# Kernel tuning notes

Hardware: AMD Instinct MI355X
Metric: run time of the kernel (lower is better)

## Reference

```python
import jax, jax.numpy as jnp
import numpy as np

B, T, N = 512, 1024, 48


def setup_inputs() -> dict:
    key = jax.random.key(0)
    k1, k2, k3, k4 = jax.random.split(key, 4)
    potentials = jax.random.normal(k1, (B, T, N), dtype=jnp.float32)
    y_true = jax.random.randint(k2, (B, T), 0, N, dtype=jnp.int32)
    lengths = jax.random.randint(k3, (B,), 1, T + 1, dtype=jnp.int32)
    transitions = jax.random.normal(k4, (N, N), dtype=jnp.float32)
    return {"potentials": potentials, "y_true": y_true,
            "lengths": lengths, "transitions": transitions}


def _crf_log_likelihood(potentials, tags, lengths, trans):
    # potentials: [B,T,N], tags: [B,T] int, lengths: [B] int, trans: [N,N]
    Bv, Tv, Nv = potentials.shape
    t_idx = jnp.arange(Tv)

    # ---- numerator: score of the given tag sequence ----
    unary = jnp.take_along_axis(potentials, tags[..., None], axis=2)[..., 0]  # [B,T]
    unary_mask = (t_idx[None, :] < lengths[:, None]).astype(potentials.dtype)
    unary_score = jnp.sum(unary * unary_mask, axis=1)  # [B]

    trans_scores = trans[tags[:, :-1], tags[:, 1:]]  # [B,T-1]
    pair_mask = (t_idx[None, 1:] < lengths[:, None]).astype(potentials.dtype)
    binary_score = jnp.sum(trans_scores * pair_mask, axis=1)  # [B]
    seq_score = unary_score + binary_score

    # ---- log partition: forward algorithm with length masking ----
    alpha0 = potentials[:, 0, :]  # [B,N]
    pots_rest = jnp.transpose(potentials[:, 1:, :], (1, 0, 2))  # [T-1,B,N]
    valid = (t_idx[1:, None] < lengths[None, :])  # [T-1,B]

    def step(alpha, inp):
        pot_t, v = inp  # [B,N], [B]
        # logsumexp over previous state: alpha[b,i] + trans[i,j]
        new_alpha = jax.nn.logsumexp(alpha[:, :, None] + trans[None, :, :], axis=1) + pot_t
        alpha = jnp.where(v[:, None], new_alpha, alpha)
        return alpha, None

    alpha_final, _ = jax.lax.scan(step, alpha0, (pots_rest, valid))
    log_norm = jax.nn.logsumexp(alpha_final, axis=-1)  # [B]

    return seq_score - log_norm


def reference(potentials, y_true, lengths, transitions):
    ll = _crf_log_likelihood(potentials, y_true.astype(jnp.int32),
                             lengths.astype(jnp.int32), transitions)
    return -ll  # per-sample NLL, shape [B]
```

## Files before the change

kernel.cpp:

```cpp
#include <hip/hip_runtime.h>
#include <cstdint>
#include <cstddef>

constexpr int Bb = 512;
constexpr int Tt = 1024;
constexpr int Nn = 48;
constexpr int SG = 16;
constexpr int NG = Bb / SG;
constexpr int Cc = 32;
constexpr int Lc = Tt / Cc;
constexpr int Wb = 32;

typedef short bf16x8 __attribute__((ext_vector_type(8)));
typedef float f32x4  __attribute__((ext_vector_type(4)));
typedef unsigned int u32x4 __attribute__((ext_vector_type(4)));

__device__ __forceinline__ unsigned int bf16_rne(float x) {
    const unsigned int u = __float_as_uint(x);
    return ((u + 0x7FFFu + ((u >> 16) & 1u)) >> 16);
}
__device__ __forceinline__ unsigned int pack2(float lo, float hi) {
    return bf16_rne(lo) | (bf16_rne(hi) << 16);
}
__device__ __forceinline__ float safe_log(float x) {
    return __logf(fmaxf(x, 1e-30f));
}

__launch_bounds__(64, 1)
__global__ void crf_fused(const float* __restrict__ pot,
                          const int*   __restrict__ ytrue,
                          const int*   __restrict__ lengths,
                          const float* __restrict__ trans,
                          float*       __restrict__ out)
{
    __shared__ float trans_lds[Nn * Nn];

    const int lane = threadIdx.x;
    const int ln   = lane & 15;
    const int q    = lane >> 4;
    const int gidx = blockIdx.x >> 5;
    const int c    = blockIdx.x & 31;
    const int s0   = gidx * SG;

    for (int i = lane; i < Nn * Nn; i += 64) trans_lds[i] = trans[i];
    __syncthreads();

    {
        const int    b    = blockIdx.x >> 1;
        const int    h    = blockIdx.x & 1;
        const int    lenb = lengths[b];
        const int*   yrow = ytrue + (size_t)b * Tt;
        const float* prow = pot + (size_t)b * Tt * Nn;
        float gold = 0.0f;
#pragma unroll
        for (int k = 0; k < Tt / 128; ++k) {
            const int   t    = h * (Tt / 2) + lane + 64 * k;
            const int   yt   = yrow[t];
            const int   ytm1 = yrow[(t > 0) ? (t - 1) : 0];
            const float u    = prow[(size_t)t * Nn + yt];
            const float tr   = trans_lds[ytm1 * Nn + yt];
            gold += (t < lenb) ? u : 0.0f;
            gold += (t >= 1 && t < lenb) ? tr : 0.0f;
        }
#pragma unroll
        for (int off = 32; off > 0; off >>= 1) gold += __shfl_xor(gold, off);
        if (lane == 0) atomicAdd(&out[b], -gold);
    }

    const int len_ln = lengths[s0 + ln];
    int lmax = len_ln;
#pragma unroll
    for (int off = 8; off > 0; off >>= 1) {
        const int o = __shfl_xor(lmax, off);
        lmax = (o > lmax) ? o : lmax;
    }

    const int start = (c == 0) ? 1 : c * Lc;
    if (c > 0 && start >= lmax) return;
    const int end = ((c + 1) * Lc < lmax) ? (c + 1) * Lc : lmax;

    bf16x8 Wf[3][2];
#pragma unroll
    for (int nt = 0; nt < 3; ++nt)
#pragma unroll
        for (int kc = 0; kc < 2; ++kc)
#pragma unroll
            for (int d = 0; d < 8; ++d) {
                int i;
                if (kc == 0) {
                    i = 16 * (d >> 2) + 4 * q + (d & 3);
                } else {
                    i = (q < 2) ? (32 + 8 * q + d) : -1;
                }
                const float v = (i >= 0) ? __expf(trans_lds[i * Nn + nt * 16 + ln]) : 0.0f;
                Wf[nt][kc][d] = (short)bf16_rne(v);
            }

    const int slA = ((2 * q) & 3) * 16 + ln;
    const int slB = slA + 16;
    const int slC = ln;

    const float* prow = pot + (size_t)(s0 + ln) * (Tt * Nn);
    const float* pp0 = prow + 0 * 16 + q * 4;
    const float* pp1 = prow + 1 * 16 + q * 4;
    const float* pp2 = prow + 2 * 16 + q * 4;

    int t0 = (c == 0) ? 1 : (start - Wb);
    if (t0 < 1) t0 = 1;

    f32x4 pin0 = *(const f32x4*)(pp0 + (size_t)(t0 - 1) * Nn);
    f32x4 pin1 = *(const f32x4*)(pp1 + (size_t)(t0 - 1) * Nn);
    f32x4 pin2 = *(const f32x4*)(pp2 + (size_t)(t0 - 1) * Nn);
    const float cb0 = __shfl(pin0[0], slC);

    float gacc = (c == 0) ? cb0 : 0.0f;
    f32x4 prev0, prev1, prev2;
#pragma unroll
    for (int r = 0; r < 4; ++r) {
        prev0[r] = __expf(pin0[r] - cb0);
        prev1[r] = __expf(pin1[r] - cb0);
        prev2[r] = __expf(pin2[r] - cb0);
    }

    unsigned int pk00 = pack2(prev0[0], prev0[1]);
    unsigned int pk01 = pack2(prev0[2], prev0[3]);
    unsigned int pk10 = pack2(prev1[0], prev1[1]);
    unsigned int pk11 = pack2(prev1[2], prev1[3]);
    unsigned int pk20 = pack2(prev2[0], prev2[1]);
    unsigned int pk21 = pack2(prev2[2], prev2[3]);
    bf16x8 Bf0 = __builtin_bit_cast(bf16x8, (u32x4){pk00, pk01, pk10, pk11});
    bf16x8 Bf1 = __builtin_bit_cast(bf16x8, (u32x4){
        (unsigned int)__shfl((int)pk20, slA), (unsigned int)__shfl((int)pk21, slA),
        (unsigned int)__shfl((int)pk20, slB), (unsigned int)__shfl((int)pk21, slB)});

    f32x4 P00, P01, P02, P10, P11, P12, P20, P21, P22, P30, P31, P32;
    {
        const size_t ta = (size_t)((t0 + 0 < Tt) ? t0 + 0 : Tt - 1) * Nn;
        const size_t tb = (size_t)((t0 + 1 < Tt) ? t0 + 1 : Tt - 1) * Nn;
        const size_t tc = (size_t)((t0 + 2 < Tt) ? t0 + 2 : Tt - 1) * Nn;
        const size_t td = (size_t)((t0 + 3 < Tt) ? t0 + 3 : Tt - 1) * Nn;
        P00 = *(const f32x4*)(pp0 + ta); P01 = *(const f32x4*)(pp1 + ta); P02 = *(const f32x4*)(pp2 + ta);
        P10 = *(const f32x4*)(pp0 + tb); P11 = *(const f32x4*)(pp1 + tb); P12 = *(const f32x4*)(pp2 + tb);
        P20 = *(const f32x4*)(pp0 + tc); P21 = *(const f32x4*)(pp1 + tc); P22 = *(const f32x4*)(pp2 + tc);
        P30 = *(const f32x4*)(pp0 + td); P31 = *(const f32x4*)(pp1 + td); P32 = *(const f32x4*)(pp2 + td);
    }
    f32x4 epv0, epv1, epv2;
#pragma unroll
    for (int r = 0; r < 4; ++r) {
        epv0[r] = __expf(P00[r]);
        epv1[r] = __expf(P01[r]);
        epv2[r] = __expf(P02[r]);
    }

    const int ksteps = ((end - t0) + 3) & ~3;

#define CRF_STEP(KK, LA0, LA1, LA2, NB0, NB1, NB2)                              \
    {                                                                           \
        const int t   = t0 + (KK);                                              \
        const size_t tld = (size_t)((t + 4 < Tt) ? (t + 4) : (Tt - 1)) * Nn;    \
        LA0 = *(const f32x4*)(pp0 + tld);                                       \
        LA1 = *(const f32x4*)(pp1 + tld);                                       \
        LA2 = *(const f32x4*)(pp2 + tld);                                       \
        f32x4 z = {0.0f, 0.0f, 0.0f, 0.0f};                                     \
        f32x4 D0 = __builtin_amdgcn_mfma_f32_16x16x32_bf16(Wf[0][0], Bf0, z, 0, 0, 0); \
        f32x4 D1 = __builtin_amdgcn_mfma_f32_16x16x32_bf16(Wf[1][0], Bf0, z, 0, 0, 0); \
        f32x4 D2 = __builtin_amdgcn_mfma_f32_16x16x32_bf16(Wf[2][0], Bf0, z, 0, 0, 0); \
        D0 = __builtin_amdgcn_mfma_f32_16x16x32_bf16(Wf[0][1], Bf1, D0, 0, 0, 0); \
        D1 = __builtin_amdgcn_mfma_f32_16x16x32_bf16(Wf[1][1], Bf1, D1, 0, 0, 0); \
        D2 = __builtin_amdgcn_mfma_f32_16x16x32_bf16(Wf[2][1], Bf1, D2, 0, 0, 0); \
        f32x4 a0, a1, a2;                                                       \
        _Pragma("unroll")                                                       \
        for (int r = 0; r < 4; ++r) {                                           \
            a0[r] = D0[r] * epv0[r];                                            \
            a1[r] = D1[r] * epv1[r];                                            \
            a2[r] = D2[r] * epv2[r];                                            \
        }                                                                       \
        const float cb = __shfl(a0[0], slC);                                    \
        const float rr = __builtin_amdgcn_rcpf(fmaxf(cb, 1e-30f));              \
        const float lg = safe_log(cb);                                          \
        gacc += ((t >= start) && (t < end) && (t + 1 < len_ln)) ? lg : 0.0f;    \
        const bool act = (t < len_ln);                                          \
        _Pragma("unroll")                                                       \
        for (int r = 0; r < 4; ++r) {                                           \
            prev0[r] = act ? a0[r] : prev0[r];                                  \
            prev1[r] = act ? a1[r] : prev1[r];                                  \
            prev2[r] = act ? a2[r] : prev2[r];                                  \
        }                                                                       \
        pk00 = pack2(prev0[0], prev0[1]);                                       \
        pk01 = pack2(prev0[2], prev0[3]);                                       \
        pk10 = pack2(prev1[0], prev1[1]);                                       \
        pk11 = pack2(prev1[2], prev1[3]);                                       \
        pk20 = pack2(prev2[0], prev2[1]);                                       \
        pk21 = pack2(prev2[2], prev2[3]);                                       \
        Bf0 = __builtin_bit_cast(bf16x8, (u32x4){pk00, pk01, pk10, pk11});      \
        Bf1 = __builtin_bit_cast(bf16x8, (u32x4){                               \
            (unsigned int)__shfl((int)pk20, slA), (unsigned int)__shfl((int)pk21, slA), \
            (unsigned int)__shfl((int)pk20, slB), (unsigned int)__shfl((int)pk21, slB)}); \
        _Pragma("unroll")                                                       \
        for (int r = 0; r < 4; ++r) {                                           \
            epv0[r] = __expf(NB0[r]) * rr;                                      \
            epv1[r] = __expf(NB1[r]) * rr;                                      \
            epv2[r] = __expf(NB2[r]) * rr;                                      \
        }                                                                       \
    }

    for (int k = 0; k < ksteps; k += 4) {
        CRF_STEP(k + 0, P00, P01, P02, P10, P11, P12);
        CRF_STEP(k + 1, P10, P11, P12, P20, P21, P22);
        CRF_STEP(k + 2, P20, P21, P22, P30, P31, P32);
        CRF_STEP(k + 3, P30, P31, P32, P00, P01, P02);
    }
#undef CRF_STEP

    float rs = prev0[0] + prev0[1] + prev0[2] + prev0[3]
             + prev1[0] + prev1[1] + prev1[2] + prev1[3]
             + prev2[0] + prev2[1] + prev2[2] + prev2[3];
    rs += __shfl_xor(rs, 16);
    rs += __shfl_xor(rs, 32);

    const bool active_chunk = (c == 0) || (c * Lc < len_ln);
    const bool last = active_chunk && (len_ln <= (c + 1) * Lc);
    const float G = gacc + (last ? safe_log(rs) : 0.0f);
    if (lane < 16) atomicAdd(&out[s0 + ln], G);
}

extern "C" void kernel_launch(void* const* d_in, const int* in_sizes, int n_in,
                              void* d_out, int out_size, void* d_ws, size_t ws_size,
                              hipStream_t stream)
{
    const float* pot   = (const float*)d_in[0];
    const int*   ytrue = (const int*)  d_in[1];
    const int*   lens  = (const int*)  d_in[2];
    const float* trans = (const float*)d_in[3];
    float*       out   = (float*)d_out;

    hipMemsetAsync(out, 0, (size_t)out_size * sizeof(float), stream);
    crf_fused<<<dim3(NG * Cc), dim3(64), 0, stream>>>(pot, ytrue, lens, trans, out);
}
```

Measured before the change: 182.0 us.

## Split sequence into 128 chunks, pack 4 waves per block, simplify step loop

Time is now split into 128 chunks of 8 steps instead of 32 chunks of 32, with a 16-step warm-up window, and four waves share one 256-thread block. The K-operand layout is rearranged so the second MFMA operand no longer needs cross-lane shuffles. The 4-deep unrolled register prefetch pipeline is replaced by a plain per-step loop that loads potentials directly. This raises parallelism and cuts the serial critical path per wave, but the warm-up becomes a larger share of each chunk, which adds redundant work, and load latency is no longer hidden by prefetch.

```diff
diff --git a/kernel.cpp b/kernel.cpp
--- a/kernel.cpp
+++ b/kernel.cpp
@@ -7,9 +7,9 @@
 constexpr int Nn = 48;
 constexpr int SG = 16;
 constexpr int NG = Bb / SG;
-constexpr int Cc = 32;
+constexpr int Cc = 128;
 constexpr int Lc = Tt / Cc;
-constexpr int Wb = 32;
+constexpr int Wb = 16;
 
 typedef short bf16x8 __attribute__((ext_vector_type(8)));
 typedef float f32x4  __attribute__((ext_vector_type(4)));
@@ -26,7 +26,7 @@
     return __logf(fmaxf(x, 1e-30f));
 }
 
-__launch_bounds__(64, 1)
+__launch_bounds__(256, 4)
 __global__ void crf_fused(const float* __restrict__ pot,
                           const int*   __restrict__ ytrue,
                           const int*   __restrict__ lengths,
@@ -35,26 +35,29 @@
 {
     __shared__ float trans_lds[Nn * Nn];
 
-    const int lane = threadIdx.x;
+    const int tid  = threadIdx.x;
+    const int lane = tid & 63;
+    const int wv   = tid >> 6;
     const int ln   = lane & 15;
     const int q    = lane >> 4;
-    const int gidx = blockIdx.x >> 5;
-    const int c    = blockIdx.x & 31;
+    const int gw   = blockIdx.x * 4 + wv;
+    const int gidx = gw & 31;
+    const int c    = gw >> 5;
     const int s0   = gidx * SG;
 
-    for (int i = lane; i < Nn * Nn; i += 64) trans_lds[i] = trans[i];
+    for (int i = tid; i < Nn * Nn; i += 256) trans_lds[i] = trans[i];
     __syncthreads();
 
     {
-        const int    b    = blockIdx.x >> 1;
-        const int    h    = blockIdx.x & 1;
+        const int    b    = gw >> 3;
+        const int    p    = gw & 7;
         const int    lenb = lengths[b];
         const int*   yrow = ytrue + (size_t)b * Tt;
         const float* prow = pot + (size_t)b * Tt * Nn;
         float gold = 0.0f;
 #pragma unroll
-        for (int k = 0; k < Tt / 128; ++k) {
-            const int   t    = h * (Tt / 2) + lane + 64 * k;
+        for (int k = 0; k < 2; ++k) {
+            const int   t    = p * 128 + lane + 64 * k;
             const int   yt   = yrow[t];
             const int   ytm1 = yrow[(t > 0) ? (t - 1) : 0];
             const float u    = prow[(size_t)t * Nn + yt];
@@ -77,7 +80,8 @@
 
     const int start = (c == 0) ? 1 : c * Lc;
     if (c > 0 && start >= lmax) return;
-    const int end = ((c + 1) * Lc < lmax) ? (c + 1) * Lc : lmax;
+    const int capE = (c + 1) * Lc;
+    const int end  = (capE < lmax) ? capE : lmax;
 
     bf16x8 Wf[3][2];
 #pragma unroll
@@ -87,20 +91,15 @@
 #pragma unroll
             for (int d = 0; d < 8; ++d) {
                 int i;
-                if (kc == 0) {
-                    i = 16 * (d >> 2) + 4 * q + (d & 3);
-                } else {
-                    i = (q < 2) ? (32 + 8 * q + d) : -1;
-                }
+                if (kc == 0) i = 16 * (d >> 2) + 4 * q + (d & 3);
+                else         i = (d < 4) ? (32 + 4 * q + d) : -1;
                 const float v = (i >= 0) ? __expf(trans_lds[i * Nn + nt * 16 + ln]) : 0.0f;
                 Wf[nt][kc][d] = (short)bf16_rne(v);
             }
-
-    const int slA = ((2 * q) & 3) * 16 + ln;
-    const int slB = slA + 16;
     const int slC = ln;
 
-    const float* prow = pot + (size_t)(s0 + ln) * (Tt * Nn);
+    const size_t ROWS = (size_t)Tt * Nn;
+    const float* prow = pot + (size_t)(s0 + ln) * ROWS;
     const float* pp0 = prow + 0 * 16 + q * 4;
     const float* pp1 = prow + 1 * 16 + q * 4;
     const float* pp2 = prow + 2 * 16 + q * 4;
@@ -129,88 +128,52 @@
     unsigned int pk20 = pack2(prev2[0], prev2[1]);
     unsigned int pk21 = pack2(prev2[2], prev2[3]);
     bf16x8 Bf0 = __builtin_bit_cast(bf16x8, (u32x4){pk00, pk01, pk10, pk11});
-    bf16x8 Bf1 = __builtin_bit_cast(bf16x8, (u32x4){
-        (unsigned int)__shfl((int)pk20, slA), (unsigned int)__shfl((int)pk21, slA),
-        (unsigned int)__shfl((int)pk20, slB), (unsigned int)__shfl((int)pk21, slB)});
-
-    f32x4 P00, P01, P02, P10, P11, P12, P20, P21, P22, P30, P31, P32;
-    {
-        const size_t ta = (size_t)((t0 + 0 < Tt) ? t0 + 0 : Tt - 1) * Nn;
-        const size_t tb = (size_t)((t0 + 1 < Tt) ? t0 + 1 : Tt - 1) * Nn;
-        const size_t tc = (size_t)((t0 + 2 < Tt) ? t0 + 2 : Tt - 1) * Nn;
-        const size_t td = (size_t)((t0 + 3 < Tt) ? t0 + 3 : Tt - 1) * Nn;
-        P00 = *(const f32x4*)(pp0 + ta); P01 = *(const f32x4*)(pp1 + ta); P02 = *(const f32x4*)(pp2 + ta);
-        P10 = *(const f32x4*)(pp0 + tb); P11 = *(const f32x4*)(pp1 + tb); P12 = *(const f32x4*)(pp2 + tb);
-        P20 = *(const f32x4*)(pp0 + tc); P21 = *(const f32x4*)(pp1 + tc); P22 = *(const f32x4*)(pp2 + tc);
-        P30 = *(const f32x4*)(pp0 + td); P31 = *(const f32x4*)(pp1 + td); P32 = *(const f32x4*)(pp2 + td);
-    }
-    f32x4 epv0, epv1, epv2;
-#pragma unroll
-    for (int r = 0; r < 4; ++r) {
-        epv0[r] = __expf(P00[r]);
-        epv1[r] = __expf(P01[r]);
-        epv2[r] = __expf(P02[r]);
-    }
-
-    const int ksteps = ((end - t0) + 3) & ~3;
-
-#define CRF_STEP(KK, LA0, LA1, LA2, NB0, NB1, NB2)                              \
-    {                                                                           \
-        const int t   = t0 + (KK);                                              \
-        const size_t tld = (size_t)((t + 4 < Tt) ? (t + 4) : (Tt - 1)) * Nn;    \
-        LA0 = *(const f32x4*)(pp0 + tld);                                       \
-        LA1 = *(const f32x4*)(pp1 + tld);                                       \
-        LA2 = *(const f32x4*)(pp2 + tld);                                       \
-        f32x4 z = {0.0f, 0.0f, 0.0f, 0.0f};                                     \
-        f32x4 D0 = __builtin_amdgcn_mfma_f32_16x16x32_bf16(Wf[0][0], Bf0, z, 0, 0, 0); \
-        f32x4 D1 = __builtin_amdgcn_mfma_f32_16x16x32_bf16(Wf[1][0], Bf0, z, 0, 0, 0); \
-        f32x4 D2 = __builtin_amdgcn_mfma_f32_16x16x32_bf16(Wf[2][0], Bf0, z, 0, 0, 0); \
-        D0 = __builtin_amdgcn_mfma_f32_16x16x32_bf16(Wf[0][1], Bf1, D0, 0, 0, 0); \
-        D1 = __builtin_amdgcn_mfma_f32_16x16x32_bf16(Wf[1][1], Bf1, D1, 0, 0, 0); \
-        D2 = __builtin_amdgcn_mfma_f32_16x16x32_bf16(Wf[2][1], Bf1, D2, 0, 0, 0); \
-        f32x4 a0, a1, a2;                                                       \
-        _Pragma("unroll")                                                       \
-        for (int r = 0; r < 4; ++r) {                                           \
-            a0[r] = D0[r] * epv0[r];                                            \
-            a1[r] = D1[r] * epv1[r];                                            \
-            a2[r] = D2[r] * epv2[r];                                            \
-        }                                                                       \
-        const float cb = __shfl(a0[0], slC);                                    \
-        const float rr = __builtin_amdgcn_rcpf(fmaxf(cb, 1e-30f));              \
-        const float lg = safe_log(cb);                                          \
-        gacc += ((t >= start) && (t < end) && (t + 1 < len_ln)) ? lg : 0.0f;    \
-        const bool act = (t < len_ln);                                          \
-        _Pragma("unroll")                                                       \
-        for (int r = 0; r < 4; ++r) {                                           \
-            prev0[r] = act ? a0[r] : prev0[r];                                  \
-            prev1[r] = act ? a1[r] : prev1[r];                                  \
-            prev2[r] = act ? a2[r] : prev2[r];                                  \
-        }                                                                       \
-        pk00 = pack2(prev0[0], prev0[1]);                                       \
-        pk01 = pack2(prev0[2], prev0[3]);                                       \
-        pk10 = pack2(prev1[0], prev1[1]);                                       \
-        pk11 = pack2(prev1[2], prev1[3]);                                       \
-        pk20 = pack2(prev2[0], prev2[1]);                                       \
-        pk21 = pack2(prev2[2], prev2[3]);                                       \
-        Bf0 = __builtin_bit_cast(bf16x8, (u32x4){pk00, pk01, pk10, pk11});      \
-        Bf1 = __builtin_bit_cast(bf16x8, (u32x4){                               \
-            (unsigned int)__shfl((int)pk20, slA), (unsigned int)__shfl((int)pk21, slA), \
-            (unsigned int)__shfl((int)pk20, slB), (unsigned int)__shfl((int)pk21, slB)}); \
-        _Pragma("unroll")                                                       \
-        for (int r = 0; r < 4; ++r) {                                           \
-            epv0[r] = __expf(NB0[r]) * rr;                                      \
-            epv1[r] = __expf(NB1[r]) * rr;                                      \
-            epv2[r] = __expf(NB2[r]) * rr;                                      \
-        }                                                                       \
-    }
-
-    for (int k = 0; k < ksteps; k += 4) {
-        CRF_STEP(k + 0, P00, P01, P02, P10, P11, P12);
-        CRF_STEP(k + 1, P10, P11, P12, P20, P21, P22);
-        CRF_STEP(k + 2, P20, P21, P22, P30, P31, P32);
-        CRF_STEP(k + 3, P30, P31, P32, P00, P01, P02);
-    }
-#undef CRF_STEP
+    bf16x8 Bf1 = __builtin_bit_cast(bf16x8, (u32x4){pk20, pk21, 0u, 0u});
+
+    float rrp = 1.0f;
+
+    for (int t = t0; t < end; ++t) {
+        const size_t to = (size_t)t * Nn;
+        const f32x4 PA = *(const f32x4*)(pp0 + to);
+        const f32x4 PB = *(const f32x4*)(pp1 + to);
+        const f32x4 PC = *(const f32x4*)(pp2 + to);
+
+        f32x4 z = {0.0f, 0.0f, 0.0f, 0.0f};
+        f32x4 D0 = __builtin_amdgcn_mfma_f32_16x16x32_bf16(Wf[0][0], Bf0, z, 0, 0, 0);
+        f32x4 D1 = __builtin_amdgcn_mfma_f32_16x16x32_bf16(Wf[1][0], Bf0, z, 0, 0, 0);
+        f32x4 D2 = __builtin_amdgcn_mfma_f32_16x16x32_bf16(Wf[2][0], Bf0, z, 0, 0, 0);
+        D0 = __builtin_amdgcn_mfma_f32_16x16x32_bf16(Wf[0][1], Bf1, D0, 0, 0, 0);
+        D1 = __builtin_amdgcn_mfma_f32_16x16x32_bf16(Wf[1][1], Bf1, D1, 0, 0, 0);
+        D2 = __builtin_amdgcn_mfma_f32_16x16x32_bf16(Wf[2][1], Bf1, D2, 0, 0, 0);
+
+        f32x4 a0, a1, a2;
+#pragma unroll
+        for (int r = 0; r < 4; ++r) {
+            a0[r] = D0[r] * (__expf(PA[r]) * rrp);
+            a1[r] = D1[r] * (__expf(PB[r]) * rrp);
+            a2[r] = D2[r] * (__expf(PC[r]) * rrp);
+        }
+        const float cb = __shfl(a0[0], slC);
+        const float rr = __builtin_amdgcn_rcpf(fmaxf(cb, 1e-30f));
+        const float lg = safe_log(cb);
+        gacc += ((t >= start) && (t + 1 < len_ln)) ? lg : 0.0f;
+        const bool act = (t < len_ln);
+#pragma unroll
+        for (int r = 0; r < 4; ++r) {
+            prev0[r] = act ? a0[r] : prev0[r];
+            prev1[r] = act ? a1[r] : prev1[r];
+            prev2[r] = act ? a2[r] : prev2[r];
+        }
+        pk00 = pack2(prev0[0], prev0[1]);
+        pk01 = pack2(prev0[2], prev0[3]);
+        pk10 = pack2(prev1[0], prev1[1]);
+        pk11 = pack2(prev1[2], prev1[3]);
+        pk20 = pack2(prev2[0], prev2[1]);
+        pk21 = pack2(prev2[2], prev2[3]);
+        Bf0 = __builtin_bit_cast(bf16x8, (u32x4){pk00, pk01, pk10, pk11});
+        Bf1 = __builtin_bit_cast(bf16x8, (u32x4){pk20, pk21, 0u, 0u});
+        rrp = rr;
+    }
 
     float rs = prev0[0] + prev0[1] + prev0[2] + prev0[3]
              + prev1[0] + prev1[1] + prev1[2] + prev1[3]
@@ -219,7 +182,7 @@
     rs += __shfl_xor(rs, 32);
 
     const bool active_chunk = (c == 0) || (c * Lc < len_ln);
-    const bool last = active_chunk && (len_ln <= (c + 1) * Lc);
+    const bool last = active_chunk && (len_ln <= capE);
     const float G = gacc + (last ? safe_log(rs) : 0.0f);
     if (lane < 16) atomicAdd(&out[s0 + ln], G);
 }
@@ -235,5 +198,5 @@
     float*       out   = (float*)d_out;
 
     hipMemsetAsync(out, 0, (size_t)out_size * sizeof(float), stream);
-    crf_fused<<<dim3(NG * Cc), dim3(64), 0, stream>>>(pot, ytrue, lens, trans, out);
-}
+    crf_fused<<<dim3(NG * Cc / 4), dim3(256), 0, stream>>>(pot, ytrue, lens, trans, out);
+}
```

Measured after the change: 186.1 us. 1.02x slower.
